# Kernel tuning notes

Measured on AMD Instinct MI355X. Metric: run time of the kernel, lower is better.

## Reference

```python
import jax, jax.numpy as jnp
import numpy as np

D_MODEL = 768
N_HEADS = 12
NUM_EXPERTS = 4
TOP_K = 2
SPAN_LEN = 64
GATE_HIDDEN = 128


def setup_inputs() -> dict:
    key = jax.random.key(0)
    ks = jax.random.split(key, 14)
    B, T, C, E = 4, 4096, D_MODEL, NUM_EXPERTS
    s = 0.02
    return {
        "hidden_states": jax.random.normal(ks[0], (B, T, C), jnp.float32),
        "Wq": jax.random.normal(ks[1], (E, C, C), jnp.float32) * s,
        "bq": jnp.zeros((E, C), jnp.float32),
        "Wk": jax.random.normal(ks[2], (E, C, C), jnp.float32) * s,
        "bk": jnp.zeros((E, C), jnp.float32),
        "Wv": jax.random.normal(ks[3], (E, C, C), jnp.float32) * s,
        "bv": jnp.zeros((E, C), jnp.float32),
        "gW1": jax.random.normal(ks[4], (GATE_HIDDEN, C), jnp.float32) * s,
        "gb1": jnp.zeros((GATE_HIDDEN,), jnp.float32),
        "gW2": jax.random.normal(ks[5], (E, GATE_HIDDEN), jnp.float32) * s,
        "gb2": jnp.zeros((E,), jnp.float32),
        "Wo": jax.random.normal(ks[6], (C, C), jnp.float32) * s,
        "bo": jnp.zeros((C,), jnp.float32),
    }


def _moe_proj(w, x, W, b):
    # per-expert projection then gate-weighted sum over experts
    # x: (B,N,S,C), W: (E,O,C), w: (B,N,E)
    proj = jnp.einsum("bnsc,eoc->ebnso", x, W)          # (E,B,N,S,C)
    out = jnp.einsum("bne,ebnso->bnso", w, proj)
    out = out + jnp.einsum("bne,eo->bno", w, b)[:, :, None, :]
    return out


def reference(hidden_states, Wq, bq, Wk, bk, Wv, bv, gW1, gb1, gW2, gb2, Wo, bo):
    B, T, C = hidden_states.shape
    S, H, E, K = SPAN_LEN, N_HEADS, NUM_EXPERTS, TOP_K
    Dh = C // H
    N = T // S  # T is a multiple of span_len -> no padding, all-ones masks
    x = hidden_states.reshape(B, N, S, C)

    # gating: mean-pool per span -> MLP -> top-k softmax scattered to E slots
    pooled = x.mean(axis=2)                                  # (B,N,C)
    h = jax.nn.relu(pooled @ gW1.T + gb1)
    logits = h @ gW2.T + gb2                                 # (B,N,E)
    vals, idx = jax.lax.top_k(logits, K)
    sm = jax.nn.softmax(vals, axis=-1)                       # (B,N,K)
    w = jnp.sum(jax.nn.one_hot(idx, E, dtype=sm.dtype) * sm[..., None], axis=-2)  # (B,N,E)
    entropy = -jnp.mean(jnp.sum(w * jnp.log(jnp.clip(w, 1e-9)), axis=-1))

    # gate-weighted expert QKV projections
    q = _moe_proj(w, x, Wq, bq).reshape(B, N, S, H, Dh)
    k = _moe_proj(w, x, Wk, bk).reshape(B, N, S, H, Dh)
    v = _moe_proj(w, x, Wv, bv).reshape(B, N, S, H, Dh)

    # per-span attention (mask is all ones; dropout in eval mode)
    scores = jnp.einsum("bnshd,bnthd->bnhst", q, k) / jnp.sqrt(jnp.float32(Dh))
    attn = jax.nn.softmax(scores, axis=-1)
    out = jnp.einsum("bnhst,bnthd->bnshd", attn, v).reshape(B, T, C)
    out = out @ Wo.T + bo
    return out, entropy
```

## Files before the change

### kernel.cpp

```cpp
#include <hip/hip_runtime.h>
#include <hip/hip_bf16.h>
#include <hip/hip_fp16.h>

typedef _Float16 f16;
typedef _Float16 f16x8 __attribute__((ext_vector_type(8)));
typedef _Float16 f16x4 __attribute__((ext_vector_type(4)));
typedef float f32x4 __attribute__((ext_vector_type(4)));

constexpr int B = 4;
constexpr int T = 4096;
constexpr int C = 768;
constexpr int NH = 12;
constexpr int DH = 64;
constexpr int E = 4;
constexpr int SPAN = 64;
constexpr int N = T / SPAN;
constexpr int BN = B * N;
constexpr int GH = 128;
constexpr int BTC = B * T * C;

constexpr int U_WE = E * C * C / 8;
constexpr int U_WO = C * C / 8;
constexpr int U_WTOT = 3 * U_WE + U_WO;

__global__ __launch_bounds__(768) void cvt_x_pool(
    const float* __restrict__ x, f16* __restrict__ x16,
    float* __restrict__ pooled) {
    int span = blockIdx.x;
    int tid = threadIdx.x;
    int u = tid % 96, rg = tid / 96;
    __shared__ float part[8][C];

    const float* xb = x + (size_t)span * SPAN * C;
    f16* xo = x16 + (size_t)span * SPAN * C;
    float a8[8] = {};
    #pragma unroll
    for (int j = 0; j < 8; ++j) {
        int r = rg * 8 + j;
        const float4* s = (const float4*)(xb + (size_t)r * C + u * 8);
        float4 A = s[0], Bv = s[1];
        f16x8 o;
        o[0] = (f16)A.x;  o[1] = (f16)A.y;  o[2] = (f16)A.z;  o[3] = (f16)A.w;
        o[4] = (f16)Bv.x; o[5] = (f16)Bv.y; o[6] = (f16)Bv.z; o[7] = (f16)Bv.w;
        *(f16x8*)(xo + (size_t)r * C + u * 8) = o;
        a8[0] += A.x;  a8[1] += A.y;  a8[2] += A.z;  a8[3] += A.w;
        a8[4] += Bv.x; a8[5] += Bv.y; a8[6] += Bv.z; a8[7] += Bv.w;
    }
    #pragma unroll
    for (int j = 0; j < 8; ++j) part[rg][u * 8 + j] = a8[j];
    __syncthreads();
    float s = 0.f;
    #pragma unroll
    for (int g = 0; g < 8; ++g) s += part[g][tid];
    pooled[(size_t)span * C + tid] = s * (1.f / 64.f);
}

__global__ void cvt_w(const float* __restrict__ Wq, const float* __restrict__ Wk,
                      const float* __restrict__ Wv, const float* __restrict__ Wo,
                      f16* __restrict__ Wq16, f16* __restrict__ Wk16,
                      f16* __restrict__ Wv16, f16* __restrict__ Wo16) {
    int i = blockIdx.x * blockDim.x + threadIdx.x;
    int stride = gridDim.x * blockDim.x;
    for (; i < U_WTOT; i += stride) {
        const float* src; f16* dst; int u;
        if (i < U_WE)               { src = Wq; dst = Wq16; u = i; }
        else if (i < 2 * U_WE)      { src = Wk; dst = Wk16; u = i - U_WE; }
        else if (i < 3 * U_WE)      { src = Wv; dst = Wv16; u = i - 2 * U_WE; }
        else                        { src = Wo; dst = Wo16; u = i - 3 * U_WE; }
        float4 a = ((const float4*)src)[2 * u];
        float4 b = ((const float4*)src)[2 * u + 1];
        f16x8 o;
        o[0] = (f16)a.x; o[1] = (f16)a.y; o[2] = (f16)a.z; o[3] = (f16)a.w;
        o[4] = (f16)b.x; o[5] = (f16)b.y; o[6] = (f16)b.z; o[7] = (f16)b.w;
        ((f16x8*)dst)[u] = o;
    }
}

__global__ __launch_bounds__(128) void gate_mlp(
    const float* __restrict__ pooled,
    const float* __restrict__ gW1, const float* __restrict__ gb1,
    const float* __restrict__ gW2, const float* __restrict__ gb2,
    int* __restrict__ eidx, float* __restrict__ ewts,
    float* __restrict__ ent_partial) {
    int span = blockIdx.x;
    int tid = threadIdx.x;
    __shared__ float pl[C];
    __shared__ float h[GH];
    __shared__ float logits[E];

    for (int c = tid; c < C; c += 128) pl[c] = pooled[(size_t)span * C + c];
    __syncthreads();

    {
        float acc = gb1[tid];
        const float* wrow = gW1 + (size_t)tid * C;
        #pragma unroll 8
        for (int c = 0; c < C; ++c) acc += pl[c] * wrow[c];
        h[tid] = acc > 0.f ? acc : 0.f;
    }
    __syncthreads();

    if (tid < E) {
        float acc = gb2[tid];
        const float* wrow = gW2 + (size_t)tid * GH;
        #pragma unroll 8
        for (int j = 0; j < GH; ++j) acc += h[j] * wrow[j];
        logits[tid] = acc;
    }
    __syncthreads();

    if (tid == 0) {
        int i0 = 0; float v0 = logits[0];
        for (int e = 1; e < E; ++e) { if (logits[e] > v0) { v0 = logits[e]; i0 = e; } }
        int i1 = -1; float v1 = -3.0e38f;
        for (int e = 0; e < E; ++e) { if (e != i0 && logits[e] > v1) { v1 = logits[e]; i1 = e; } }
        float bq_ = expf(v1 - v0);
        float s = 1.f + bq_;
        float sm0 = 1.f / s;
        float sm1 = bq_ / s;
        eidx[span * 2 + 0] = i0;
        eidx[span * 2 + 1] = i1;
        ewts[span * 2 + 0] = sm0;
        ewts[span * 2 + 1] = sm1;
        float p0 = fmaxf(sm0, 1e-9f), p1 = fmaxf(sm1, 1e-9f);
        ent_partial[span] = sm0 * logf(p0) + sm1 * logf(p1);
    }
}

__global__ void entropy_kernel(const float* __restrict__ ent_partial, float* __restrict__ out_ent) {
    __shared__ float sh[256];
    int tid = threadIdx.x;
    sh[tid] = ent_partial[tid];
    __syncthreads();
    for (int s = 128; s > 0; s >>= 1) {
        if (tid < s) sh[tid] += sh[tid + s];
        __syncthreads();
    }
    if (tid == 0) *out_ent = -sh[0] * (1.0f / (float)BN);
}

constexpr int QNCH = 24;

__global__ __launch_bounds__(256, 3) void qkv_mfma(
    const f16* __restrict__ xh,
    const f16* __restrict__ Wq16, const float* __restrict__ bq,
    const f16* __restrict__ Wk16, const float* __restrict__ bk,
    const f16* __restrict__ Wv16, const float* __restrict__ bv,
    const int* __restrict__ eidx, const float* __restrict__ ewts,
    f16* __restrict__ q16, f16* __restrict__ k16, f16* __restrict__ vt)
{
    int span  = blockIdx.x;
    int otile = blockIdx.y;
    int proj  = blockIdx.z;

    const f16* W; const float* bias; f16* out;
    if (proj == 0)      { W = Wq16; bias = bq; out = q16; }
    else if (proj == 1) { W = Wk16; bias = bk; out = k16; }
    else                { W = Wv16; bias = bv; out = vt; }

    int e0 = eidx[span * 2 + 0], e1 = eidx[span * 2 + 1];
    float w0 = ewts[span * 2 + 0], w1 = ewts[span * 2 + 1];
    f16 w0h = (f16)w0, w1h = (f16)w1;

    __shared__ __align__(16) f16 xs[64 * 40];
    __shared__ __align__(16) f16 ws[256 * 40];

    int tid = threadIdx.x;
    int lane = tid & 63, wv = tid >> 6;
    int lr = lane & 15, lg = lane >> 4;

    int srow = tid >> 2, su = tid & 3;

    const char* xp  = (const char*)xh + ((size_t)span * 64 + srow) * 1536 + su * 16;
    const char* w0p[4]; const char* w1p[4];
    {
        const char* wb0 = (const char*)W + ((size_t)e0 * C + otile * 256 + srow) * 1536 + su * 16;
        const char* wb1 = (const char*)W + ((size_t)e1 * C + otile * 256 + srow) * 1536 + su * 16;
        #pragma unroll
        for (int i = 0; i < 4; ++i) {
            w0p[i] = wb0 + (size_t)i * 64 * 1536;
            w1p[i] = wb1 + (size_t)i * 64 * 1536;
        }
    }

    f16* xw = &xs[srow * 40 + su * 8];
    f16* ww = &ws[srow * 40 + su * 8];

    const f16* ar[4]; const f16* br[4];
    #pragma unroll
    for (int m = 0; m < 4; ++m) ar[m] = &xs[(m * 16 + lr) * 40 + lg * 8];
    #pragma unroll
    for (int n = 0; n < 4; ++n) br[n] = &ws[(wv * 64 + n * 16 + lr) * 40 + lg * 8];

    f32x4 acc[4][4] = {};

    f16x8 xr, w0r[4], w1r[4];
    xr = *(const f16x8*)xp;
    #pragma unroll
    for (int i = 0; i < 4; ++i) {
        w0r[i] = *(const f16x8*)w0p[i];
        w1r[i] = *(const f16x8*)w1p[i];
    }

    for (int ch = 0; ch < QNCH; ++ch) {
        *(f16x8*)xw = xr;
        #pragma unroll
        for (int i = 0; i < 4; ++i)
            *(f16x8*)(ww + i * 2560) = w0r[i] * w0h + w1r[i] * w1h;

        if (ch < QNCH - 1) {
            xp += 64;
            xr = *(const f16x8*)xp;
            #pragma unroll
            for (int i = 0; i < 4; ++i) {
                w0p[i] += 64; w1p[i] += 64;
                w0r[i] = *(const f16x8*)w0p[i];
                w1r[i] = *(const f16x8*)w1p[i];
            }
        }

        asm volatile("s_waitcnt lgkmcnt(0)" ::: "memory");
        __builtin_amdgcn_s_barrier();
        __builtin_amdgcn_sched_barrier(0);

        f16x8 af[4], bf[4];
        #pragma unroll
        for (int m = 0; m < 4; ++m) af[m] = *(const f16x8*)ar[m];
        #pragma unroll
        for (int n = 0; n < 4; ++n) bf[n] = *(const f16x8*)br[n];
        __builtin_amdgcn_s_setprio(1);
        #pragma unroll
        for (int m = 0; m < 4; ++m)
            #pragma unroll
            for (int n = 0; n < 4; ++n)
                acc[m][n] = __builtin_amdgcn_mfma_f32_16x16x32_f16(af[m], bf[n], acc[m][n], 0, 0, 0);
        __builtin_amdgcn_s_setprio(0);

        asm volatile("s_waitcnt lgkmcnt(0)" ::: "memory");
        __builtin_amdgcn_s_barrier();
        __builtin_amdgcn_sched_barrier(0);
    }

    if (proj == 2) {
        f16* vtb = out + (size_t)span * C * 64;
        #pragma unroll
        for (int n = 0; n < 4; ++n) {
            int col = otile * 256 + wv * 64 + n * 16 + lr;
            float be = w0 * bias[(size_t)e0 * C + col] + w1 * bias[(size_t)e1 * C + col];
            #pragma unroll
            for (int m = 0; m < 4; ++m) {
                f16x4 pk;
                #pragma unroll
                for (int r = 0; r < 4; ++r) pk[r] = (f16)(acc[m][n][r] + be);
                *(f16x4*)&vtb[(size_t)col * 64 + m * 16 + lg * 4] = pk;
            }
        }
    } else {
        f16* outb = out + (size_t)span * 64 * C;
        #pragma unroll
        for (int n = 0; n < 4; ++n) {
            int col = otile * 256 + wv * 64 + n * 16 + lr;
            float be = w0 * bias[(size_t)e0 * C + col] + w1 * bias[(size_t)e1 * C + col];
            #pragma unroll
            for (int m = 0; m < 4; ++m) {
                #pragma unroll
                for (int r = 0; r < 4; ++r) {
                    int row = m * 16 + lg * 4 + r;
                    outb[(size_t)row * C + col] = (f16)(acc[m][n][r] + be);
                }
            }
        }
    }
}

__global__ __launch_bounds__(256) void attn_mfma(
    const f16* __restrict__ q16, const f16* __restrict__ k16,
    const f16* __restrict__ vt, f16* __restrict__ a16)
{
    int h = blockIdx.x, span = blockIdx.y;
    __shared__ __align__(16) f16 Klds[64 * 72];
    __shared__ __align__(16) f16 Vlds[64 * 72];
    __shared__ __align__(16) f16 Plds[64 * 72];

    int tid = threadIdx.x;
    int lane = tid & 63, mt = tid >> 6;
    int lr = lane & 15, lg = lane >> 4;

    const f16x8* ku = (const f16x8*)k16;
    const f16x8* vu = (const f16x8*)vt;
    #pragma unroll
    for (int i = 0; i < 2; ++i) {
        int id = tid + i * 256;
        int r = id >> 3, u = id & 7;
        *(f16x8*)&Klds[r * 72 + u * 8] = ku[(size_t)span * 6144 + (size_t)r * 96 + h * 8 + u];
        *(f16x8*)&Vlds[r * 72 + u * 8] = vu[(size_t)span * 6144 + (size_t)(h * 64 + r) * 8 + u];
    }
    __syncthreads();

    const f16x8* qu = (const f16x8*)q16;
    f16x8 qa[2];
    #pragma unroll
    for (int kk = 0; kk < 2; ++kk)
        qa[kk] = qu[(size_t)span * 6144 + (size_t)(mt * 16 + lr) * 96 + h * 8 + kk * 4 + lg];

    f32x4 accs[4] = {};
    #pragma unroll
    for (int nt = 0; nt < 4; ++nt) {
        #pragma unroll
        for (int kk = 0; kk < 2; ++kk) {
            f16x8 kb = *(const f16x8*)&Klds[(nt * 16 + lr) * 72 + kk * 32 + lg * 8];
            accs[nt] = __builtin_amdgcn_mfma_f32_16x16x32_f16(qa[kk], kb, accs[nt], 0, 0, 0);
        }
    }

    #pragma unroll
    for (int nt = 0; nt < 4; ++nt) accs[nt] *= 0.125f;
    f32x4 m4;
    #pragma unroll
    for (int r = 0; r < 4; ++r)
        m4[r] = fmaxf(fmaxf(accs[0][r], accs[1][r]), fmaxf(accs[2][r], accs[3][r]));
    #pragma unroll
    for (int st = 1; st < 16; st <<= 1) {
        #pragma unroll
        for (int r = 0; r < 4; ++r) m4[r] = fmaxf(m4[r], __shfl_xor(m4[r], st));
    }
    f32x4 ps[4];
    f32x4 sum4 = {0.f, 0.f, 0.f, 0.f};
    #pragma unroll
    for (int nt = 0; nt < 4; ++nt)
        #pragma unroll
        for (int r = 0; r < 4; ++r) {
            ps[nt][r] = __expf(accs[nt][r] - m4[r]);
            sum4[r] += ps[nt][r];
        }
    #pragma unroll
    for (int st = 1; st < 16; st <<= 1) {
        #pragma unroll
        for (int r = 0; r < 4; ++r) sum4[r] += __shfl_xor(sum4[r], st);
    }
    f32x4 inv4;
    #pragma unroll
    for (int r = 0; r < 4; ++r) inv4[r] = 1.0f / sum4[r];

    #pragma unroll
    for (int nt = 0; nt < 4; ++nt)
        #pragma unroll
        for (int r = 0; r < 4; ++r)
            Plds[(mt * 16 + lg * 4 + r) * 72 + nt * 16 + lr] = (f16)ps[nt][r];
    __syncthreads();

    f16x8 pa[2];
    #pragma unroll
    for (int kkt = 0; kkt < 2; ++kkt)
        pa[kkt] = *(const f16x8*)&Plds[(mt * 16 + lr) * 72 + kkt * 32 + lg * 8];
    f32x4 acco[4] = {};
    #pragma unroll
    for (int nt = 0; nt < 4; ++nt) {
        #pragma unroll
        for (int kkt = 0; kkt < 2; ++kkt) {
            f16x8 vb = *(const f16x8*)&Vlds[(nt * 16 + lr) * 72 + kkt * 32 + lg * 8];
            acco[nt] = __builtin_amdgcn_mfma_f32_16x16x32_f16(pa[kkt], vb, acco[nt], 0, 0, 0);
        }
    }

    #pragma unroll
    for (int nt = 0; nt < 4; ++nt)
        #pragma unroll
        for (int r = 0; r < 4; ++r)
            Klds[(mt * 16 + lg * 4 + r) * 72 + nt * 16 + lr] = (f16)(acco[nt][r] * inv4[r]);
    __syncthreads();

    int row = mt * 16 + (lane >> 2);
    int u2 = (lane & 3) * 2;
    f16x8 o0 = *(const f16x8*)&Klds[row * 72 + u2 * 8];
    f16x8 o1 = *(const f16x8*)&Klds[row * 72 + u2 * 8 + 8];
    f16x8* au = (f16x8*)a16;
    au[(size_t)span * 6144 + (size_t)row * 96 + h * 8 + u2]     = o0;
    au[(size_t)span * 6144 + (size_t)row * 96 + h * 8 + u2 + 1] = o1;
}

__global__ __launch_bounds__(512) void outproj_mfma(
    const f16* __restrict__ ah, const f16* __restrict__ Wo16,
    const float* __restrict__ bo, float* __restrict__ Y)
{
    int rt = blockIdx.x;
    int otile = blockIdx.y;

    __shared__ f16x8 as_u[128 * 8];
    __shared__ f16x8 ws_u[256 * 8];

    const f16x8* au  = (const f16x8*)(ah + (size_t)rt * 128 * C);
    const f16x8* Wou = (const f16x8*)(Wo16 + (size_t)otile * 256 * C);

    int tid = threadIdx.x;
    int lane = tid & 63, wv = tid >> 6;
    int lr = lane & 15, lg = lane >> 4;
    int wm = (wv >> 2) * 64;
    int wn = (wv & 3) * 64;

    f32x4 acc[4][4] = {};

    for (int kc8 = 0; kc8 < 96; kc8 += 8) {
        #pragma unroll
        for (int i = 0; i < 2; ++i) {
            int id = tid + i * 512;
            int r = id >> 3, u = id & 7;
            as_u[r * 8 + (u ^ (r & 7))] = au[(size_t)r * 96 + kc8 + u];
        }
        #pragma unroll
        for (int i = 0; i < 4; ++i) {
            int id = tid + i * 512;
            int r = id >> 3, u = id & 7;
            ws_u[r * 8 + (u ^ (r & 7))] = Wou[(size_t)r * 96 + kc8 + u];
        }
        __syncthreads();
        #pragma unroll
        for (int kk = 0; kk < 2; ++kk) {
            int ub = kk * 4 + lg;
            f16x8 afrag[4], bfrag[4];
            #pragma unroll
            for (int m = 0; m < 4; ++m) {
                int r = wm + m * 16 + lr;
                afrag[m] = as_u[r * 8 + (ub ^ (r & 7))];
            }
            #pragma unroll
            for (int n = 0; n < 4; ++n) {
                int r = wn + n * 16 + lr;
                bfrag[n] = ws_u[r * 8 + (ub ^ (r & 7))];
            }
            #pragma unroll
            for (int m = 0; m < 4; ++m)
                #pragma unroll
                for (int n = 0; n < 4; ++n)
                    acc[m][n] = __builtin_amdgcn_mfma_f32_16x16x32_f16(afrag[m], bfrag[n], acc[m][n], 0, 0, 0);
        }
        __syncthreads();
    }

    #pragma unroll
    for (int n = 0; n < 4; ++n) {
        int col = otile * 256 + wn + n * 16 + lr;
        float be = bo[col];
        #pragma unroll
        for (int m = 0; m < 4; ++m) {
            #pragma unroll
            for (int r = 0; r < 4; ++r) {
                int row = rt * 128 + wm + m * 16 + lg * 4 + r;
                Y[(size_t)row * C + col] = acc[m][n][r] + be;
            }
        }
    }
}

extern "C" void kernel_launch(void* const* d_in, const int* in_sizes, int n_in,
                              void* d_out, int out_size, void* d_ws, size_t ws_size,
                              hipStream_t stream) {
    const float* x   = (const float*)d_in[0];
    const float* Wq  = (const float*)d_in[1];
    const float* bq  = (const float*)d_in[2];
    const float* Wk  = (const float*)d_in[3];
    const float* bk  = (const float*)d_in[4];
    const float* Wv  = (const float*)d_in[5];
    const float* bv  = (const float*)d_in[6];
    const float* gW1 = (const float*)d_in[7];
    const float* gb1 = (const float*)d_in[8];
    const float* gW2 = (const float*)d_in[9];
    const float* gb2 = (const float*)d_in[10];
    const float* Wo  = (const float*)d_in[11];
    const float* bo  = (const float*)d_in[12];

    float* out = (float*)d_out;

    char* ws = (char*)d_ws;
    const size_t h_btc = (size_t)BTC * sizeof(f16);
    f16* x16  = (f16*)(ws);
    f16* q16  = (f16*)(ws + 1 * h_btc);
    f16* k16  = (f16*)(ws + 2 * h_btc);
    f16* vt16 = (f16*)(ws + 3 * h_btc);
    f16* a16  = (f16*)(ws + 4 * h_btc);
    size_t off = 5 * h_btc;
    const size_t wsz = (size_t)E * C * C * sizeof(f16);
    f16* Wq16 = (f16*)(ws + off); off += wsz;
    f16* Wk16 = (f16*)(ws + off); off += wsz;
    f16* Wv16 = (f16*)(ws + off); off += wsz;
    f16* Wo16 = (f16*)(ws + off); off += (size_t)C * C * sizeof(f16);
    int*   eidx = (int*)(ws + off); off += 2048;
    float* ewts = (float*)(ws + off); off += 2048;
    float* entp = (float*)(ws + off); off += 1024;
    float* pooled = (float*)(ws + off); off += (size_t)BN * C * sizeof(float);

    cvt_x_pool<<<dim3(BN), dim3(768), 0, stream>>>(x, x16, pooled);
    cvt_w<<<dim3(1024), dim3(256), 0, stream>>>(Wq, Wk, Wv, Wo,
                                                Wq16, Wk16, Wv16, Wo16);
    gate_mlp<<<dim3(BN), dim3(128), 0, stream>>>(pooled, gW1, gb1, gW2, gb2,
                                                 eidx, ewts, entp);
    entropy_kernel<<<dim3(1), dim3(256), 0, stream>>>(entp, out + BTC);

    qkv_mfma<<<dim3(BN, 3, 3), dim3(256), 0, stream>>>(x16, Wq16, bq, Wk16, bk, Wv16, bv,
                                                       eidx, ewts, q16, k16, vt16);
    attn_mfma<<<dim3(NH, BN), dim3(256), 0, stream>>>(q16, k16, vt16, a16);
    outproj_mfma<<<dim3(128, 3), dim3(512), 0, stream>>>(a16, Wo16, bo, out);
}
```

Baseline: 251.3 us.

## Pair spans sharing the same expert pair to reuse weight loads in QKV projection

A new kernel groups spans by their unordered top-2 expert pair and packs them two per slot. Each QKV block then processes two spans that share expert weights, loading the two experts' weight tiles once and building a separately mixed weight tile for each span. The output tile shrinks from 256 to 128 columns, and the LDS layout switches to an XOR-swizzled 64-wide k-chunk. This halves global weight traffic per span, at the cost of an extra serial kernel, a grid sized for the worst case whose unused blocks exit early, and wasted work in slots holding a lone span.

```diff
diff --git a/kernel.cpp b/kernel.cpp
--- a/kernel.cpp
+++ b/kernel.cpp
@@ -139,7 +139,43 @@
     if (tid == 0) *out_ent = -sh[0] * (1.0f / (float)BN);
 }
 
-constexpr int QNCH = 24;
+constexpr int MAXSLOTS = 131;
+
+__global__ __launch_bounds__(256) void pair_spans(
+    const int* __restrict__ eidx,
+    int* __restrict__ slotA, int* __restrict__ slotB, int* __restrict__ nslots)
+{
+    __shared__ int cnt[16];
+    __shared__ int base[16];
+    __shared__ int pos[16];
+    __shared__ int list[256];
+    int t = threadIdx.x;
+    if (t < 16) cnt[t] = 0;
+    __syncthreads();
+    int a = eidx[t * 2], b = eidx[t * 2 + 1];
+    int lo = a < b ? a : b, hi = a < b ? b : a;
+    int key = lo * 4 + hi;
+    atomicAdd(&cnt[key], 1);
+    __syncthreads();
+    if (t == 0) {
+        int acc = 0;
+        for (int k = 0; k < 16; ++k) { base[k] = acc; pos[k] = acc; acc += cnt[k]; }
+    }
+    __syncthreads();
+    int p = atomicAdd(&pos[key], 1);
+    list[p] = t;
+    __syncthreads();
+    if (t == 0) {
+        int ns = 0;
+        for (int k = 0; k < 16; ++k) {
+            int s = base[k], c = cnt[k];
+            int i = 0;
+            for (; i + 1 < c; i += 2) { slotA[ns] = list[s + i]; slotB[ns] = list[s + i + 1]; ++ns; }
+            if (i < c) { slotA[ns] = list[s + i]; slotB[ns] = -1; ++ns; }
+        }
+        *nslots = ns;
+    }
+}
 
 __global__ __launch_bounds__(256, 3) void qkv_mfma(
     const f16* __restrict__ xh,
@@ -147,9 +183,12 @@
     const f16* __restrict__ Wk16, const float* __restrict__ bk,
     const f16* __restrict__ Wv16, const float* __restrict__ bv,
     const int* __restrict__ eidx, const float* __restrict__ ewts,
+    const int* __restrict__ slotA, const int* __restrict__ slotB,
+    const int* __restrict__ nslots,
     f16* __restrict__ q16, f16* __restrict__ k16, f16* __restrict__ vt)
 {
-    int span  = blockIdx.x;
+    int slot = blockIdx.x;
+    if (slot >= *nslots) return;
     int otile = blockIdx.y;
     int proj  = blockIdx.z;
 
@@ -158,95 +197,107 @@
     else if (proj == 1) { W = Wk16; bias = bk; out = k16; }
     else                { W = Wv16; bias = bv; out = vt; }
 
-    int e0 = eidx[span * 2 + 0], e1 = eidx[span * 2 + 1];
-    float w0 = ewts[span * 2 + 0], w1 = ewts[span * 2 + 1];
-    f16 w0h = (f16)w0, w1h = (f16)w1;
-
-    __shared__ __align__(16) f16 xs[64 * 40];
-    __shared__ __align__(16) f16 ws[256 * 40];
+    int spA = slotA[slot];
+    int spBr = slotB[slot];
+    bool isPair = spBr >= 0;
+    int spB = isPair ? spBr : spA;
+
+    int a0 = eidx[spA * 2], a1 = eidx[spA * 2 + 1];
+    int ea = a0 < a1 ? a0 : a1, eb = a0 < a1 ? a1 : a0;
+    float wA0 = ewts[spA * 2], wA1 = ewts[spA * 2 + 1];
+    float wAa = (a0 == ea) ? wA0 : wA1;
+    float wAb = (a0 == ea) ? wA1 : wA0;
+    int b0 = eidx[spB * 2];
+    float wB0 = ewts[spB * 2], wB1 = ewts[spB * 2 + 1];
+    float wBa = (b0 == ea) ? wB0 : wB1;
+    float wBb = (b0 == ea) ? wB1 : wB0;
+    f16 wAah = (f16)wAa, wAbh = (f16)wAb, wBah = (f16)wBa, wBbh = (f16)wBb;
+
+    __shared__ f16x8 xs[2 * 512];
+    __shared__ f16x8 wsm[2 * 1024];
 
     int tid = threadIdx.x;
     int lane = tid & 63, wv = tid >> 6;
     int lr = lane & 15, lg = lane >> 4;
-
-    int srow = tid >> 2, su = tid & 3;
-
-    const char* xp  = (const char*)xh + ((size_t)span * 64 + srow) * 1536 + su * 16;
-    const char* w0p[4]; const char* w1p[4];
-    {
-        const char* wb0 = (const char*)W + ((size_t)e0 * C + otile * 256 + srow) * 1536 + su * 16;
-        const char* wb1 = (const char*)W + ((size_t)e1 * C + otile * 256 + srow) * 1536 + su * 16;
+    int sp = wv & 1, cg = wv >> 1;
+
+    int prow = tid >> 3, pu = tid & 7;
+    int psw = pu ^ (prow & 7);
+
+    const f16x8* xuA = (const f16x8*)(xh + (size_t)spA * 64 * C) + (size_t)prow * 96 + pu;
+    const f16x8* xuB = (const f16x8*)(xh + (size_t)spB * 64 * C) + (size_t)prow * 96 + pu;
+    const f16x8* wpa = (const f16x8*)(W + ((size_t)ea * C + otile * 128) * C) + (size_t)prow * 96 + pu;
+    const f16x8* wpb = (const f16x8*)(W + ((size_t)eb * C + otile * 128) * C) + (size_t)prow * 96 + pu;
+
+    f32x4 acc[4][4] = {};
+
+    f16x8 xA0, xA1, xB0, xB1, wa[4], wb[4];
+    xA0 = xuA[0]; xA1 = xuA[3072];
+    xB0 = xuB[0]; xB1 = xuB[3072];
+    #pragma unroll
+    for (int i = 0; i < 4; ++i) { wa[i] = wpa[(size_t)i * 3072]; wb[i] = wpb[(size_t)i * 3072]; }
+
+    for (int ch = 0; ch < 12; ++ch) {
+        xs[prow * 8 + psw]          = xA0;
+        xs[(prow + 32) * 8 + psw]   = xA1;
+        xs[512 + prow * 8 + psw]        = xB0;
+        xs[512 + (prow + 32) * 8 + psw] = xB1;
         #pragma unroll
         for (int i = 0; i < 4; ++i) {
-            w0p[i] = wb0 + (size_t)i * 64 * 1536;
-            w1p[i] = wb1 + (size_t)i * 64 * 1536;
-        }
-    }
-
-    f16* xw = &xs[srow * 40 + su * 8];
-    f16* ww = &ws[srow * 40 + su * 8];
-
-    const f16* ar[4]; const f16* br[4];
-    #pragma unroll
-    for (int m = 0; m < 4; ++m) ar[m] = &xs[(m * 16 + lr) * 40 + lg * 8];
-    #pragma unroll
-    for (int n = 0; n < 4; ++n) br[n] = &ws[(wv * 64 + n * 16 + lr) * 40 + lg * 8];
-
-    f32x4 acc[4][4] = {};
-
-    f16x8 xr, w0r[4], w1r[4];
-    xr = *(const f16x8*)xp;
-    #pragma unroll
-    for (int i = 0; i < 4; ++i) {
-        w0r[i] = *(const f16x8*)w0p[i];
-        w1r[i] = *(const f16x8*)w1p[i];
-    }
-
-    for (int ch = 0; ch < QNCH; ++ch) {
-        *(f16x8*)xw = xr;
-        #pragma unroll
-        for (int i = 0; i < 4; ++i)
-            *(f16x8*)(ww + i * 2560) = w0r[i] * w0h + w1r[i] * w1h;
-
-        if (ch < QNCH - 1) {
-            xp += 64;
-            xr = *(const f16x8*)xp;
-            #pragma unroll
-            for (int i = 0; i < 4; ++i) {
-                w0p[i] += 64; w1p[i] += 64;
-                w0r[i] = *(const f16x8*)w0p[i];
-                w1r[i] = *(const f16x8*)w1p[i];
-            }
+            int r = prow + i * 32;
+            wsm[r * 8 + psw]        = wa[i] * wAah + wb[i] * wAbh;
+            wsm[1024 + r * 8 + psw] = wa[i] * wBah + wb[i] * wBbh;
+        }
+
+        if (ch < 11) {
+            xuA += 8; xuB += 8; wpa += 8; wpb += 8;
+            xA0 = xuA[0]; xA1 = xuA[3072];
+            xB0 = xuB[0]; xB1 = xuB[3072];
+            #pragma unroll
+            for (int i = 0; i < 4; ++i) { wa[i] = wpa[(size_t)i * 3072]; wb[i] = wpb[(size_t)i * 3072]; }
         }
 
         asm volatile("s_waitcnt lgkmcnt(0)" ::: "memory");
         __builtin_amdgcn_s_barrier();
         __builtin_amdgcn_sched_barrier(0);
 
-        f16x8 af[4], bf[4];
-        #pragma unroll
-        for (int m = 0; m < 4; ++m) af[m] = *(const f16x8*)ar[m];
-        #pragma unroll
-        for (int n = 0; n < 4; ++n) bf[n] = *(const f16x8*)br[n];
-        __builtin_amdgcn_s_setprio(1);
-        #pragma unroll
-        for (int m = 0; m < 4; ++m)
-            #pragma unroll
-            for (int n = 0; n < 4; ++n)
-                acc[m][n] = __builtin_amdgcn_mfma_f32_16x16x32_f16(af[m], bf[n], acc[m][n], 0, 0, 0);
-        __builtin_amdgcn_s_setprio(0);
+        #pragma unroll
+        for (int kk = 0; kk < 2; ++kk) {
+            int ub = kk * 4 + lg;
+            f16x8 af[4], bf[4];
+            #pragma unroll
+            for (int m = 0; m < 4; ++m) {
+                int r = m * 16 + lr;
+                af[m] = xs[sp * 512 + r * 8 + (ub ^ (r & 7))];
+            }
+            #pragma unroll
+            for (int n = 0; n < 4; ++n) {
+                int r = cg * 64 + n * 16 + lr;
+                bf[n] = wsm[sp * 1024 + r * 8 + (ub ^ (r & 7))];
+            }
+            #pragma unroll
+            for (int m = 0; m < 4; ++m)
+                #pragma unroll
+                for (int n = 0; n < 4; ++n)
+                    acc[m][n] = __builtin_amdgcn_mfma_f32_16x16x32_f16(af[m], bf[n], acc[m][n], 0, 0, 0);
+        }
 
         asm volatile("s_waitcnt lgkmcnt(0)" ::: "memory");
         __builtin_amdgcn_s_barrier();
         __builtin_amdgcn_sched_barrier(0);
     }
 
+    if (sp == 1 && !isPair) return;
+    int span = sp ? spB : spA;
+    float wwa = sp ? wBa : wAa;
+    float wwb = sp ? wBb : wAb;
+
     if (proj == 2) {
         f16* vtb = out + (size_t)span * C * 64;
         #pragma unroll
         for (int n = 0; n < 4; ++n) {
-            int col = otile * 256 + wv * 64 + n * 16 + lr;
-            float be = w0 * bias[(size_t)e0 * C + col] + w1 * bias[(size_t)e1 * C + col];
+            int col = otile * 128 + cg * 64 + n * 16 + lr;
+            float be = wwa * bias[(size_t)ea * C + col] + wwb * bias[(size_t)eb * C + col];
             #pragma unroll
             for (int m = 0; m < 4; ++m) {
                 f16x4 pk;
@@ -259,8 +310,8 @@
         f16* outb = out + (size_t)span * 64 * C;
         #pragma unroll
         for (int n = 0; n < 4; ++n) {
-            int col = otile * 256 + wv * 64 + n * 16 + lr;
-            float be = w0 * bias[(size_t)e0 * C + col] + w1 * bias[(size_t)e1 * C + col];
+            int col = otile * 128 + cg * 64 + n * 16 + lr;
+            float be = wwa * bias[(size_t)ea * C + col] + wwb * bias[(size_t)eb * C + col];
             #pragma unroll
             for (int m = 0; m < 4; ++m) {
                 #pragma unroll
@@ -488,16 +539,21 @@
     float* ewts = (float*)(ws + off); off += 2048;
     float* entp = (float*)(ws + off); off += 1024;
     float* pooled = (float*)(ws + off); off += (size_t)BN * C * sizeof(float);
+    int* slotA  = (int*)(ws + off); off += 1024;
+    int* slotB  = (int*)(ws + off); off += 1024;
+    int* nslots = (int*)(ws + off); off += 256;
 
     cvt_x_pool<<<dim3(BN), dim3(768), 0, stream>>>(x, x16, pooled);
     cvt_w<<<dim3(1024), dim3(256), 0, stream>>>(Wq, Wk, Wv, Wo,
                                                 Wq16, Wk16, Wv16, Wo16);
     gate_mlp<<<dim3(BN), dim3(128), 0, stream>>>(pooled, gW1, gb1, gW2, gb2,
                                                  eidx, ewts, entp);
+    pair_spans<<<dim3(1), dim3(256), 0, stream>>>(eidx, slotA, slotB, nslots);
     entropy_kernel<<<dim3(1), dim3(256), 0, stream>>>(entp, out + BTC);
 
-    qkv_mfma<<<dim3(BN, 3, 3), dim3(256), 0, stream>>>(x16, Wq16, bq, Wk16, bk, Wv16, bv,
-                                                       eidx, ewts, q16, k16, vt16);
+    qkv_mfma<<<dim3(MAXSLOTS, 6, 3), dim3(256), 0, stream>>>(
+        x16, Wq16, bq, Wk16, bk, Wv16, bv,
+        eidx, ewts, slotA, slotB, nslots, q16, k16, vt16);
     attn_mfma<<<dim3(NH, BN), dim3(256), 0, stream>>>(q16, k16, vt16, a16);
     outproj_mfma<<<dim3(128, 3), dim3(512), 0, stream>>>(a16, Wo16, bo, out);
 }
```

New measurement: 222.2 us. 11.6% less time.
